# Performance work log

Measured on AMD Instinct MI355X. Metric: run time of the kernel, lower is better.

Reference implementation:

```python
import jax, jax.numpy as jnp
import numpy as np

B, N_ANT, M_MEAS, D_A, MAX_ITER = 1024, 64, 16, 4096, 20
SC_L = 10


def setup_inputs() -> dict:
    key = jax.random.key(0)
    ks = jax.random.split(key, 9)
    return {
        "x_re": jax.random.normal(ks[0], (B, M_MEAS), jnp.float32),
        "x_im": jax.random.normal(ks[1], (B, M_MEAS), jnp.float32),
        "xm_re": jax.random.normal(ks[2], (B, N_ANT), jnp.float32),
        "xm_im": jax.random.normal(ks[3], (B, N_ANT), jnp.float32),
        "M_re": jax.random.normal(ks[4], (B, N_ANT, M_MEAS), jnp.float32),
        "M_im": jax.random.normal(ks[5], (B, N_ANT, M_MEAS), jnp.float32),
        "W_re": jax.random.normal(ks[6], (N_ANT, D_A), jnp.float32),
        "W_im": jax.random.normal(ks[7], (N_ANT, D_A), jnp.float32),
        "sigma": jax.random.uniform(ks[8], (B,), jnp.float32) * 0.05,
        "L": SC_L,
        "k": 1,
    }


def _mpnet_forward(x, xm, M, W, sigma, L):
    # M_D[b] = conj(M[b]^T) @ W  -> [B, m, d_a]
    M_D = jnp.einsum('bnm,na->bma', jnp.conj(M), W)
    # per-sample column normalization (norms are constants: torch computes them on detached numpy)
    md_norm = jax.lax.stop_gradient(
        jnp.sqrt(jnp.sum(jnp.abs(M_D) ** 2, axis=1, keepdims=True)))  # [B,1,d_a]
    M_D = M_D / md_norm
    e_norm = jax.lax.stop_gradient(
        jnp.sqrt(jnp.sum(jnp.abs(W) ** 2, axis=0, keepdims=True)))  # [1,d_a]
    E = W / e_norm  # [N, d_a]

    n_full = xm.shape[1]
    threshold = (sigma ** 2) * n_full * L  # sc == 2

    def body(carry, _):
        residual, res, active = carry
        rn2 = jnp.sum(jnp.abs(residual) ** 2, axis=1)         # [B]
        active = active & (rn2 >= threshold)                  # per-sample early exit
        corr = jnp.einsum('bm,bma->ba', residual, jnp.conj(M_D))  # [B,d_a]
        idx = jnp.argmax(jnp.abs(corr), axis=1)               # top-1 (keep_k_max, k=1)
        val = jnp.take_along_axis(corr, idx[:, None], axis=1)           # [B,1]
        col = jnp.take_along_axis(M_D, idx[:, None, None], axis=2)[..., 0]  # [B,m]
        colE = jnp.take(E, idx, axis=1).T                     # [B,N]
        residual = jnp.where(active[:, None], residual - val * col, residual)
        res = jnp.where(active[:, None], res - val * colE, res)
        return (residual, res, active), None

    init = (x, xm, jnp.ones((x.shape[0],), dtype=bool))
    (residual, res, _), _ = jax.lax.scan(body, init, None, length=MAX_ITER)
    x_hat = x - residual
    x_hat_m = xm - res
    return residual, x_hat, x_hat_m


def reference(x_re, x_im, xm_re, xm_im, M_re, M_im, W_re, W_im, sigma, L, k):
    x = (x_re + 1j * x_im).astype(jnp.complex64)
    xm = (xm_re + 1j * xm_im).astype(jnp.complex64)
    M = (M_re + 1j * M_im).astype(jnp.complex64)
    W = (W_re + 1j * W_im).astype(jnp.complex64)
    return _mpnet_forward(x, xm, M, W, sigma, L)
```

## Files before the change

### kernel.cpp

```cpp
#include <hip/hip_runtime.h>
#include <cstdint>
#include <cstddef>

#define NB_TOT 1024
#define NANT 64
#define MM 16
#define MPAD 17
#define DA 4096
#define MAXIT 20
#define SPB 4
#define NTHR 1024
#define JCOLS 4
#define L_CONST 10.0f

__global__ __launch_bounds__(NTHR, 4)
void mpnet_kernel(const float* __restrict__ x_re, const float* __restrict__ x_im,
                  const float* __restrict__ xm_re, const float* __restrict__ xm_im,
                  const float* __restrict__ M_re, const float* __restrict__ M_im,
                  const float* __restrict__ W_re, const float* __restrict__ W_im,
                  const float* __restrict__ sigma,
                  float* __restrict__ out, int outn_i)
{
  __shared__ float Msh_re[SPB][NANT][MPAD];
  __shared__ float Msh_im[SPB][NANT][MPAD];
  __shared__ float md_T[SPB][JCOLS][NTHR];
  __shared__ float tsh[NANT][8];
  __shared__ float rsd_re[SPB][MM], rsd_im[SPB][MM];
  __shared__ float resh_re[SPB][NANT], resh_im[SPB][NANT];
  __shared__ float red_c2[16][SPB];
  __shared__ int   red_ix[16][SPB];
  __shared__ int   sel_ix[SPB];
  __shared__ float sel_vr[SPB], sel_vi[SPB], sel_md[SPB], sel_ei[SPB];
  __shared__ float rn2_sh[SPB], thr_sh[SPB];
  __shared__ int   actsh[SPB];

  const int tid = threadIdx.x;
  const int b0 = blockIdx.x * SPB;
  const size_t outn = (size_t)outn_i;

  for (int k2 = 0; k2 < 4; k2++){
    int idx = k2*NTHR + tid;
    int s = idx >> 10, rem = idx & 1023;
    int n = rem >> 4, m = rem & 15;
    Msh_re[s][n][m] = M_re[(size_t)b0*1024 + idx];
    Msh_im[s][n][m] = M_im[(size_t)b0*1024 + idx];
  }
  if (tid < SPB*MM){
    int s = tid >> 4, m = tid & 15;
    rsd_re[s][m] = x_re[(b0+s)*MM + m];
    rsd_im[s][m] = x_im[(b0+s)*MM + m];
  } else if (tid >= 64 && tid < 64 + SPB*NANT){
    int q = tid - 64, s = q >> 6, n = q & 63;
    resh_re[s][n] = xm_re[(b0+s)*NANT + n];
    resh_im[s][n] = xm_im[(b0+s)*NANT + n];
  } else if (tid >= 448 && tid < 448 + SPB){
    int s = tid - 448;
    float sg = sigma[b0+s];
    thr_sh[s] = ((sg*sg) * (float)NANT) * L_CONST;
    actsh[s] = 1;
  }

  #pragma unroll
  for (int s = 0; s < SPB; s++){
    const float* MrS = M_re + (size_t)(b0+s)*1024;
    const float* MiS = M_im + (size_t)(b0+s)*1024;
    #pragma unroll
    for (int jc = 0; jc < 2; jc++){
      float nrm0 = 0.f, nrm1 = 0.f;
      #pragma unroll
      for (int mc = 0; mc < 2; mc++){
        float cr0[8], ci0[8], cr1[8], ci1[8];
        #pragma unroll
        for (int q = 0; q < 8; q++){ cr0[q]=0.f; ci0[q]=0.f; cr1[q]=0.f; ci1[q]=0.f; }
        #pragma unroll 4
        for (int n = 0; n < NANT; n++){
          float2 w_r = *(const float2*)(W_re + (size_t)n*DA + (tid<<2) + jc*2);
          float2 w_i = *(const float2*)(W_im + (size_t)n*DA + (tid<<2) + jc*2);
          const float* Mr = MrS + n*MM + mc*8;
          const float* Mi = MiS + n*MM + mc*8;
          #pragma unroll
          for (int q = 0; q < 8; q++){
            float mr = Mr[q], mi = Mi[q];
            cr0[q] += mr*w_r.x + mi*w_i.x;  ci0[q] += mr*w_i.x - mi*w_r.x;
            cr1[q] += mr*w_r.y + mi*w_i.y;  ci1[q] += mr*w_i.y - mi*w_r.y;
          }
        }
        #pragma unroll
        for (int q = 0; q < 8; q++){
          nrm0 += cr0[q]*cr0[q] + ci0[q]*ci0[q];
          nrm1 += cr1[q]*cr1[q] + ci1[q]*ci1[q];
        }
      }
      md_T[s][jc*2+0][tid] = 1.f/sqrtf(nrm0);
      md_T[s][jc*2+1][tid] = 1.f/sqrtf(nrm1);
    }
  }
  __syncthreads();

  for (int it = 0; it < MAXIT; it++){
    if (tid < SPB){
      float e = 0.f;
      for (int m = 0; m < MM; m++){
        float rr = rsd_re[tid][m], ri = rsd_im[tid][m];
        e += rr*rr + ri*ri;
      }
      rn2_sh[tid] = e;
    } else if (tid >= 64 && tid < 320){
      int q = tid - 64, s = q >> 6, n = q & 63;
      if (actsh[s]){
        float tr = 0.f, ti = 0.f;
        #pragma unroll
        for (int m = 0; m < MM; m++){
          float mr = Msh_re[s][n][m], mi = Msh_im[s][n][m];
          float rr = rsd_re[s][m], ri = rsd_im[s][m];
          tr += mr*rr - mi*ri;
          ti += mr*ri + mi*rr;
        }
        tsh[n][2*s]   = tr;
        tsh[n][2*s+1] = ti;
      }
    }
    __syncthreads();

    bool a0 = actsh[0] && (rn2_sh[0] >= thr_sh[0]);
    bool a1 = actsh[1] && (rn2_sh[1] >= thr_sh[1]);
    bool a2 = actsh[2] && (rn2_sh[2] >= thr_sh[2]);
    bool a3 = actsh[3] && (rn2_sh[3] >= thr_sh[3]);
    if (tid < 4){
      int v = (tid==0) ? (int)a0 : (tid==1) ? (int)a1 : (tid==2) ? (int)a2 : (int)a3;
      actsh[tid] = v;
    }
    if (!(a0 || a1 || a2 || a3)) break;

    float gr[SPB][JCOLS], gi[SPB][JCOLS];
    #pragma unroll
    for (int s = 0; s < SPB; s++)
      #pragma unroll
      for (int j = 0; j < JCOLS; j++){ gr[s][j]=0.f; gi[s][j]=0.f; }
    #pragma unroll 8
    for (int n = 0; n < NANT; n++){
      float4 t01 = *(const float4*)&tsh[n][0];
      float4 t23 = *(const float4*)&tsh[n][4];
      float4 wr = *(const float4*)(W_re + (size_t)n*DA + (tid<<2));
      float4 wi = *(const float4*)(W_im + (size_t)n*DA + (tid<<2));
      if (a0){
        gr[0][0] += wr.x*t01.x + wi.x*t01.y;  gi[0][0] += wr.x*t01.y - wi.x*t01.x;
        gr[0][1] += wr.y*t01.x + wi.y*t01.y;  gi[0][1] += wr.y*t01.y - wi.y*t01.x;
        gr[0][2] += wr.z*t01.x + wi.z*t01.y;  gi[0][2] += wr.z*t01.y - wi.z*t01.x;
        gr[0][3] += wr.w*t01.x + wi.w*t01.y;  gi[0][3] += wr.w*t01.y - wi.w*t01.x;
      }
      if (a1){
        gr[1][0] += wr.x*t01.z + wi.x*t01.w;  gi[1][0] += wr.x*t01.w - wi.x*t01.z;
        gr[1][1] += wr.y*t01.z + wi.y*t01.w;  gi[1][1] += wr.y*t01.w - wi.y*t01.z;
        gr[1][2] += wr.z*t01.z + wi.z*t01.w;  gi[1][2] += wr.z*t01.w - wi.z*t01.z;
        gr[1][3] += wr.w*t01.z + wi.w*t01.w;  gi[1][3] += wr.w*t01.w - wi.w*t01.z;
      }
      if (a2){
        gr[2][0] += wr.x*t23.x + wi.x*t23.y;  gi[2][0] += wr.x*t23.y - wi.x*t23.x;
        gr[2][1] += wr.y*t23.x + wi.y*t23.y;  gi[2][1] += wr.y*t23.y - wi.y*t23.x;
        gr[2][2] += wr.z*t23.x + wi.z*t23.y;  gi[2][2] += wr.z*t23.y - wi.z*t23.x;
        gr[2][3] += wr.w*t23.x + wi.w*t23.y;  gi[2][3] += wr.w*t23.y - wi.w*t23.x;
      }
      if (a3){
        gr[3][0] += wr.x*t23.z + wi.x*t23.w;  gi[3][0] += wr.x*t23.w - wi.x*t23.z;
        gr[3][1] += wr.y*t23.z + wi.y*t23.w;  gi[3][1] += wr.y*t23.w - wi.y*t23.z;
        gr[3][2] += wr.z*t23.z + wi.z*t23.w;  gi[3][2] += wr.z*t23.w - wi.z*t23.z;
        gr[3][3] += wr.w*t23.z + wi.w*t23.w;  gi[3][3] += wr.w*t23.w - wi.w*t23.z;
      }
    }

    const bool acts[4] = {a0, a1, a2, a3};
    float bc2[SPB]; int bix[SPB];
    #pragma unroll
    for (int s = 0; s < SPB; s++){
      bc2[s] = -1.f; bix[s] = 0;
      if (acts[s]){
        float m0 = md_T[s][0][tid], m1 = md_T[s][1][tid];
        float m2 = md_T[s][2][tid], m3 = md_T[s][3][tid];
        float c0 = (gr[s][0]*gr[s][0] + gi[s][0]*gi[s][0]) * (m0*m0);
        float c1 = (gr[s][1]*gr[s][1] + gi[s][1]*gi[s][1]) * (m1*m1);
        float c2v = (gr[s][2]*gr[s][2] + gi[s][2]*gi[s][2]) * (m2*m2);
        float c3 = (gr[s][3]*gr[s][3] + gi[s][3]*gi[s][3]) * (m3*m3);
        float bc = c0; int bi = (tid<<2);
        if (c1 > bc){ bc = c1; bi = (tid<<2)+1; }
        if (c2v > bc){ bc = c2v; bi = (tid<<2)+2; }
        if (c3 > bc){ bc = c3; bi = (tid<<2)+3; }
        bc2[s] = bc; bix[s] = bi;
      }
    }
    #pragma unroll
    for (int s = 0; s < SPB; s++){
      if (acts[s]){
        #pragma unroll
        for (int off = 32; off; off >>= 1){
          float oc2 = __shfl_down(bc2[s], off);
          int   oix = __shfl_down(bix[s], off);
          if (oc2 > bc2[s] || (oc2 == bc2[s] && oix < bix[s])){ bc2[s]=oc2; bix[s]=oix; }
        }
      }
    }
    if ((tid & 63) == 0){
      int wid = tid >> 6;
      #pragma unroll
      for (int s = 0; s < SPB; s++){
        if (acts[s]){ red_c2[wid][s]=bc2[s]; red_ix[wid][s]=bix[s]; }
      }
    }
    __syncthreads();

    if (tid < 256){
      int s = tid >> 6, lane = tid & 63;
      if (actsh[s]){
        float c = (lane < 16) ? red_c2[lane][s] : -1.f;
        int   bi = (lane < 16) ? red_ix[lane][s] : 0x7FFFFFFF;
        #pragma unroll
        for (int off = 8; off; off >>= 1){
          float oc = __shfl_down(c, off);
          int   oi = __shfl_down(bi, off);
          if (oc > c || (oc == c && oi < bi)){ c = oc; bi = oi; }
        }
        int I = __shfl(bi, 0);
        float wr = W_re[(size_t)lane*DA + I], wi = W_im[(size_t)lane*DA + I];
        float tr = tsh[lane][2*s], ti = tsh[lane][2*s+1];
        float vr = wr*tr + wi*ti;
        float vi = wr*ti - wi*tr;
        float w2 = wr*wr + wi*wi;
        #pragma unroll
        for (int off = 32; off; off >>= 1){
          vr += __shfl_down(vr, off);
          vi += __shfl_down(vi, off);
          w2 += __shfl_down(w2, off);
        }
        if (lane == 0){
          float mdv = md_T[s][I & 3][I >> 2];
          sel_ix[s] = I;
          sel_vr[s] = vr*mdv;
          sel_vi[s] = vi*mdv;
          sel_md[s] = mdv;
          sel_ei[s] = rsqrtf(w2);
        }
      }
    }
    __syncthreads();

    if (tid < 64){
      int s = tid >> 4, m = tid & 15;
      if (actsh[s]){
        int I = sel_ix[s];
        float vr = sel_vr[s], vi = sel_vi[s], mdv = sel_md[s];
        float cre = 0.f, cim = 0.f;
        for (int n = 0; n < NANT; n++){
          float mr = Msh_re[s][n][m], mi = Msh_im[s][n][m];
          float wr = W_re[(size_t)n*DA + I], wi = W_im[(size_t)n*DA + I];
          cre += mr*wr + mi*wi;
          cim += mr*wi - mi*wr;
        }
        cre *= mdv; cim *= mdv;
        rsd_re[s][m] -= vr*cre - vi*cim;
        rsd_im[s][m] -= vr*cim + vi*cre;
      }
    } else if (tid >= 64 && tid < 320){
      int q = tid - 64, s = q >> 6, n = q & 63;
      if (actsh[s]){
        int I = sel_ix[s];
        float vr = sel_vr[s], vi = sel_vi[s];
        float wr = W_re[(size_t)n*DA + I], wi = W_im[(size_t)n*DA + I];
        float ei = sel_ei[s];
        float er = wr*ei, em = wi*ei;
        resh_re[s][n] -= vr*er - vi*em;
        resh_im[s][n] -= vr*em + vi*er;
      }
    }
    __syncthreads();
  }

  if (tid < 64){
    int s = tid >> 4, m = tid & 15; int b = b0 + s;
    float rr = rsd_re[s][m], ri = rsd_im[s][m];
    size_t base = (size_t)b*MM + m;
    if (base < outn)          out[base]          = rr;
    if (16384 + base < outn)  out[16384 + base]  = x_re[b*MM+m] - rr;
    if (98304 + base < outn)  out[98304 + base]  = ri;
    if (114688 + base < outn) out[114688 + base] = x_im[b*MM+m] - ri;
  } else if (tid >= 64 && tid < 320){
    int q = tid - 64, s = q >> 6, n = q & 63; int b = b0 + s;
    size_t base = (size_t)b*NANT + n;
    if (32768 + base < outn)  out[32768 + base]  = xm_re[b*NANT+n] - resh_re[s][n];
    if (131072 + base < outn) out[131072 + base] = xm_im[b*NANT+n] - resh_im[s][n];
  }
}

extern "C" void kernel_launch(void* const* d_in, const int* in_sizes, int n_in,
                              void* d_out, int out_size, void* d_ws, size_t ws_size,
                              hipStream_t stream) {
  (void)in_sizes; (void)n_in; (void)d_ws; (void)ws_size;
  const float* x_re  = (const float*)d_in[0];
  const float* x_im  = (const float*)d_in[1];
  const float* xm_re = (const float*)d_in[2];
  const float* xm_im = (const float*)d_in[3];
  const float* M_re  = (const float*)d_in[4];
  const float* M_im  = (const float*)d_in[5];
  const float* W_re  = (const float*)d_in[6];
  const float* W_im  = (const float*)d_in[7];
  const float* sig   = (const float*)d_in[8];
  float* out = (float*)d_out;

  dim3 grid(NB_TOT / SPB), block(NTHR);
  hipLaunchKernelGGL(mpnet_kernel, grid, block, 0, stream,
                     x_re, x_im, xm_re, xm_im, M_re, M_im, W_re, W_im,
                     sig, out, out_size);
}
```

Before: 1.531 ms.

## Fuse selection and residual update into one wave per sample, restructure norm precompute

The per-sample selection wave now performs the residual and res updates directly with butterfly (xor) shuffles, which removes the sel_* shared buffers and one block-wide barrier per iteration. The selected column is computed by a 64-lane reduction for each of the 16 measurements instead of a serial 64-step loop that re-read W from global memory. The column-norm precompute is rewritten to process one column at a time with all 16 measurements in registers and float4 loads of M. This trades more shuffles per iteration and more register pressure in the precompute for fewer barriers and fewer global reads.

```diff
diff --git a/kernel.cpp b/kernel.cpp
--- a/kernel.cpp
+++ b/kernel.cpp
@@ -29,8 +29,6 @@
   __shared__ float resh_re[SPB][NANT], resh_im[SPB][NANT];
   __shared__ float red_c2[16][SPB];
   __shared__ int   red_ix[16][SPB];
-  __shared__ int   sel_ix[SPB];
-  __shared__ float sel_vr[SPB], sel_vi[SPB], sel_md[SPB], sel_ei[SPB];
   __shared__ float rn2_sh[SPB], thr_sh[SPB];
   __shared__ int   actsh[SPB];
 
@@ -65,34 +63,31 @@
     const float* MrS = M_re + (size_t)(b0+s)*1024;
     const float* MiS = M_im + (size_t)(b0+s)*1024;
     #pragma unroll
-    for (int jc = 0; jc < 2; jc++){
-      float nrm0 = 0.f, nrm1 = 0.f;
-      #pragma unroll
-      for (int mc = 0; mc < 2; mc++){
-        float cr0[8], ci0[8], cr1[8], ci1[8];
-        #pragma unroll
-        for (int q = 0; q < 8; q++){ cr0[q]=0.f; ci0[q]=0.f; cr1[q]=0.f; ci1[q]=0.f; }
-        #pragma unroll 4
-        for (int n = 0; n < NANT; n++){
-          float2 w_r = *(const float2*)(W_re + (size_t)n*DA + (tid<<2) + jc*2);
-          float2 w_i = *(const float2*)(W_im + (size_t)n*DA + (tid<<2) + jc*2);
-          const float* Mr = MrS + n*MM + mc*8;
-          const float* Mi = MiS + n*MM + mc*8;
-          #pragma unroll
-          for (int q = 0; q < 8; q++){
-            float mr = Mr[q], mi = Mi[q];
-            cr0[q] += mr*w_r.x + mi*w_i.x;  ci0[q] += mr*w_i.x - mi*w_r.x;
-            cr1[q] += mr*w_r.y + mi*w_i.y;  ci1[q] += mr*w_i.y - mi*w_r.y;
-          }
-        }
-        #pragma unroll
-        for (int q = 0; q < 8; q++){
-          nrm0 += cr0[q]*cr0[q] + ci0[q]*ci0[q];
-          nrm1 += cr1[q]*cr1[q] + ci1[q]*ci1[q];
-        }
-      }
-      md_T[s][jc*2+0][tid] = 1.f/sqrtf(nrm0);
-      md_T[s][jc*2+1][tid] = 1.f/sqrtf(nrm1);
+    for (int jc = 0; jc < JCOLS; jc++){
+      const int col = (tid<<2) + jc;
+      float cr[MM], ci[MM];
+      #pragma unroll
+      for (int q = 0; q < MM; q++){ cr[q]=0.f; ci[q]=0.f; }
+      #pragma unroll 2
+      for (int n = 0; n < NANT; n++){
+        float wr = W_re[(size_t)n*DA + col];
+        float wi = W_im[(size_t)n*DA + col];
+        const float* Mr = MrS + n*MM;
+        const float* Mi = MiS + n*MM;
+        #pragma unroll
+        for (int q2 = 0; q2 < 4; q2++){
+          float4 m4r = *(const float4*)(Mr + q2*4);
+          float4 m4i = *(const float4*)(Mi + q2*4);
+          cr[q2*4+0] += m4r.x*wr + m4i.x*wi;  ci[q2*4+0] += m4r.x*wi - m4i.x*wr;
+          cr[q2*4+1] += m4r.y*wr + m4i.y*wi;  ci[q2*4+1] += m4r.y*wi - m4i.y*wr;
+          cr[q2*4+2] += m4r.z*wr + m4i.z*wi;  ci[q2*4+2] += m4r.z*wi - m4i.z*wr;
+          cr[q2*4+3] += m4r.w*wr + m4i.w*wi;  ci[q2*4+3] += m4r.w*wi - m4i.w*wr;
+        }
+      }
+      float nrm = 0.f;
+      #pragma unroll
+      for (int q = 0; q < MM; q++) nrm += cr[q]*cr[q] + ci[q]*ci[q];
+      md_T[s][jc][tid] = 1.f/sqrtf(nrm);
     }
   }
   __syncthreads();
@@ -100,6 +95,7 @@
   for (int it = 0; it < MAXIT; it++){
     if (tid < SPB){
       float e = 0.f;
+      #pragma unroll
       for (int m = 0; m < MM; m++){
         float rr = rsd_re[tid][m], ri = rsd_im[tid][m];
         e += rr*rr + ri*ri;
@@ -215,8 +211,8 @@
         int   bi = (lane < 16) ? red_ix[lane][s] : 0x7FFFFFFF;
         #pragma unroll
         for (int off = 8; off; off >>= 1){
-          float oc = __shfl_down(c, off);
-          int   oi = __shfl_down(bi, off);
+          float oc = __shfl_xor(c, off);
+          int   oi = __shfl_xor(bi, off);
           if (oc > c || (oc == c && oi < bi)){ c = oc; bi = oi; }
         }
         int I = __shfl(bi, 0);
@@ -227,48 +223,31 @@
         float w2 = wr*wr + wi*wi;
         #pragma unroll
         for (int off = 32; off; off >>= 1){
-          vr += __shfl_down(vr, off);
-          vi += __shfl_down(vi, off);
-          w2 += __shfl_down(w2, off);
-        }
-        if (lane == 0){
-          float mdv = md_T[s][I & 3][I >> 2];
-          sel_ix[s] = I;
-          sel_vr[s] = vr*mdv;
-          sel_vi[s] = vi*mdv;
-          sel_md[s] = mdv;
-          sel_ei[s] = rsqrtf(w2);
-        }
-      }
-    }
-    __syncthreads();
-
-    if (tid < 64){
-      int s = tid >> 4, m = tid & 15;
-      if (actsh[s]){
-        int I = sel_ix[s];
-        float vr = sel_vr[s], vi = sel_vi[s], mdv = sel_md[s];
-        float cre = 0.f, cim = 0.f;
-        for (int n = 0; n < NANT; n++){
-          float mr = Msh_re[s][n][m], mi = Msh_im[s][n][m];
-          float wr = W_re[(size_t)n*DA + I], wi = W_im[(size_t)n*DA + I];
-          cre += mr*wr + mi*wi;
-          cim += mr*wi - mi*wr;
-        }
-        cre *= mdv; cim *= mdv;
-        rsd_re[s][m] -= vr*cre - vi*cim;
-        rsd_im[s][m] -= vr*cim + vi*cre;
-      }
-    } else if (tid >= 64 && tid < 320){
-      int q = tid - 64, s = q >> 6, n = q & 63;
-      if (actsh[s]){
-        int I = sel_ix[s];
-        float vr = sel_vr[s], vi = sel_vi[s];
-        float wr = W_re[(size_t)n*DA + I], wi = W_im[(size_t)n*DA + I];
-        float ei = sel_ei[s];
-        float er = wr*ei, em = wi*ei;
-        resh_re[s][n] -= vr*er - vi*em;
-        resh_im[s][n] -= vr*em + vi*er;
+          vr += __shfl_xor(vr, off);
+          vi += __shfl_xor(vi, off);
+          w2 += __shfl_xor(w2, off);
+        }
+        float mdv = md_T[s][I & 3][I >> 2];
+        float val_r = vr*mdv, val_i = vi*mdv;
+        float einv = rsqrtf(w2);
+        float er = wr*einv, em = wi*einv;
+        resh_re[s][lane] -= val_r*er - val_i*em;
+        resh_im[s][lane] -= val_r*em + val_i*er;
+        for (int m = 0; m < MM; m++){
+          float mr = Msh_re[s][lane][m], mi = Msh_im[s][lane][m];
+          float pr = mr*wr + mi*wi;
+          float pi = mr*wi - mi*wr;
+          #pragma unroll
+          for (int off = 32; off; off >>= 1){
+            pr += __shfl_xor(pr, off);
+            pi += __shfl_xor(pi, off);
+          }
+          if (lane == m){
+            float col_r = pr*mdv, col_i = pi*mdv;
+            rsd_re[s][m] -= val_r*col_r - val_i*col_i;
+            rsd_im[s][m] -= val_r*col_i + val_i*col_r;
+          }
+        }
       }
     }
     __syncthreads();
```

After: 1.418 ms. 7.4% less time.
